# Performance work log

Hardware: AMD Instinct MI355X
Metric: run time of the kernel (lower is better)

## Reference

```python
import jax, jax.numpy as jnp
import numpy as np

N = 100000   # nodes
C = 128      # in_channels
K = 32       # n_super_nodes
B = 64       # graphs (num segments)


def setup_inputs() -> dict:
    key = jax.random.key(0)
    k_x, k_b, k_w1, k_b1, k_w2, k_b2 = jax.random.split(key, 6)
    x = jax.random.normal(k_x, (N, C), dtype=jnp.float32)
    batch = jnp.sort(jax.random.randint(k_b, (N,), 0, B))
    # assign_mlp params: Linear(C,C) -> ReLU -> Linear(C,K); stored as [in,out]
    W1 = jax.random.normal(k_w1, (C, C), dtype=jnp.float32) / np.sqrt(C)
    b1 = jax.random.normal(k_b1, (C,), dtype=jnp.float32) * 0.01
    W2 = jax.random.normal(k_w2, (C, K), dtype=jnp.float32) / np.sqrt(C)
    b2 = jax.random.normal(k_b2, (K,), dtype=jnp.float32) * 0.01
    return {"x": x, "batch": batch, "W1": W1, "b1": b1, "W2": W2, "b2": b2}


def reference(x, batch, W1, b1, W2, b2):
    # assignment logits: MLP over node features
    h = jax.nn.relu(x @ W1 + b1)          # [N, C]
    s = jax.nn.softmax(h @ W2 + b2, axis=-1)  # [N, K]
    # outer product per node, then scatter-sum by graph id
    x_expanded = x[:, None, :] * s[:, :, None]  # [N, K, C]
    out = jax.ops.segment_sum(x_expanded, batch, num_segments=B)  # [B, K, C]
    return (out, s)
```

## Files before the change

### kernel.cpp

```cpp
#include <hip/hip_runtime.h>
#include <hip/hip_bf16.h>

#define NN 100000
#define CC 128
#define KK 32
#define BB 64
#define CH 4
#define NCHUNK (NN / 32)
#define NSLOT 16

typedef __bf16 bf16x8 __attribute__((ext_vector_type(8)));
typedef float  f32x4  __attribute__((ext_vector_type(4)));

__device__ __forceinline__ unsigned short f2bf(float v) {
    union { __bf16 h; unsigned short s; } u;
    u.h = (__bf16)v;
    return u.s;
}
__device__ __forceinline__ float bf2f(unsigned short h) {
    union { unsigned u; float f; } a; a.u = ((unsigned)h) << 16;
    return a.f;
}
__device__ __forceinline__ void unpack_hilo(uint4 a, uint4 b,
                                            bf16x8& hi8, bf16x8& lo8) {
    union { unsigned u[4]; bf16x8 v; } H, L;
    H.u[0] = __builtin_amdgcn_perm(a.y, a.x, 0x05040100u);
    H.u[1] = __builtin_amdgcn_perm(a.w, a.z, 0x05040100u);
    H.u[2] = __builtin_amdgcn_perm(b.y, b.x, 0x05040100u);
    H.u[3] = __builtin_amdgcn_perm(b.w, b.z, 0x05040100u);
    L.u[0] = __builtin_amdgcn_perm(a.y, a.x, 0x07060302u);
    L.u[1] = __builtin_amdgcn_perm(a.w, a.z, 0x07060302u);
    L.u[2] = __builtin_amdgcn_perm(b.y, b.x, 0x07060302u);
    L.u[3] = __builtin_amdgcn_perm(b.w, b.z, 0x07060302u);
    hi8 = H.v; lo8 = L.v;
}

__global__ __launch_bounds__(256) void hp_prep(const int* __restrict__ batch,
                                               const float* __restrict__ W1,
                                               const float* __restrict__ W2,
                                               int* __restrict__ bounds,
                                               unsigned short* __restrict__ w1f,
                                               unsigned short* __restrict__ w2f,
                                               float* __restrict__ part) {
    if (blockIdx.x == 0 && threadIdx.x <= BB) {
        const int b = threadIdx.x;
        int lo = 0, hi = NN;
        while (lo < hi) {
            const int mid = (lo + hi) >> 1;
            if (batch[mid] < b) lo = mid + 1; else hi = mid;
        }
        bounds[b] = lo;
    }
    const int t = blockIdx.x * 256 + threadIdx.x;
    if (t < 16384) {
        const int idx  = t;
        const int j    = idx & 7;
        const int lane = (idx >> 3) & 63;
        const int nt   = (idx >> 9) & 7;
        const int kt   = idx >> 12;
        const int k = kt * 32 + (lane >> 4) * 8 + j;
        const int n = nt * 16 + (lane & 15);
        const float w = W1[k * CC + n];
        const unsigned short h = f2bf(w);
        w1f[idx]         = h;
        w1f[16384 + idx] = f2bf(w - bf2f(h));
    }
    if (t < 4096) {
        const int idx  = t;
        const int j    = idx & 7;
        const int lane = (idx >> 3) & 63;
        const int nt   = (idx >> 9) & 1;
        const int kt   = idx >> 10;
        const int k = kt * 32 + (lane >> 4) * 8 + j;
        const int n = nt * 16 + (lane & 15);
        const float w = W2[k * KK + n];
        const unsigned short h = f2bf(w);
        w2f[idx]        = h;
        w2f[4096 + idx] = f2bf(w - bf2f(h));
    }
    const float4 z = make_float4(0.f, 0.f, 0.f, 0.f);
    for (int i = t; i < BB * NSLOT * KK * CC / 4; i += 65536)
        *(float4*)(part + (size_t)i * 4) = z;
}

__global__ __launch_bounds__(256, 3) void hp_fused(
    const float* __restrict__ x,
    const unsigned short* __restrict__ w1f,
    const unsigned short* __restrict__ w2f,
    const float* __restrict__ b1,
    const float* __restrict__ b2,
    const int* __restrict__ batch,
    const int* __restrict__ bounds,
    float* __restrict__ s_out,
    float* __restrict__ part)
{
    __shared__ __align__(16) char uni[16896];
    __shared__ __align__(16) unsigned short xbL[8 * 64 * 8];
    __shared__ float lgT[32][36];
    __shared__ float redm[4][32];
    __shared__ float reds[4][32];

    unsigned short* xa   = (unsigned short*)uni;
    unsigned int*   hs16 = (unsigned int*)uni;

    const int t    = threadIdx.x;
    const int wave = __builtin_amdgcn_readfirstlane(t >> 6);
    const int lane = t & 63;

    const int pmt   = wave & 1;
    const int chalf = wave >> 1;
    const int nrow  = (lane >> 4) * 8;

    f32x4 pacc[4];
    #pragma unroll
    for (int i = 0; i < 4; ++i) pacc[i] = (f32x4){0.f, 0.f, 0.f, 0.f};

    int cg = __builtin_amdgcn_readfirstlane(batch[blockIdx.x * (CH * 32)]);

    auto flush = [&](int g) {
        const int slot = blockIdx.x - (bounds[g] >> 7);
        float* op = part + ((size_t)g * NSLOT + slot) * (KK * CC);
        #pragma unroll
        for (int i = 0; i < 4; ++i) {
            const int c = (chalf * 4 + i) * 16 + (lane & 15);
            #pragma unroll
            for (int r = 0; r < 4; ++r) {
                const int k = pmt * 16 + (lane >> 4) * 4 + r;
                op[k * CC + c] = pacc[i][r];
            }
            pacc[i] = (f32x4){0.f, 0.f, 0.f, 0.f};
        }
    };

    #pragma unroll 1
    for (int ch = 0; ch < CH; ++ch) {
        const int chunk = blockIdx.x * CH + ch;
        if (chunk >= NCHUNK) break;
        const int base = chunk * 32;

        __syncthreads();

        #pragma unroll
        for (int mt = 0; mt < 2; ++mt) {
            const int q  = mt * 4 + wave;
            const int n  = base + mt * 16 + (lane & 15);
            const int ck = wave * 32 + (lane >> 4) * 8;
            const float4 va = *(const float4*)(x + (size_t)n * CC + ck);
            const float4 vb = *(const float4*)(x + (size_t)n * CC + ck + 4);
            const float v[8] = {va.x, va.y, va.z, va.w, vb.x, vb.y, vb.z, vb.w};
            union { unsigned short s[8]; uint4 u; } H, L;
            #pragma unroll
            for (int j = 0; j < 8; ++j) {
                H.s[j] = f2bf(v[j]);
                L.s[j] = f2bf(v[j] - bf2f(H.s[j]));
            }
            unsigned short* d0 = xa + (q * 64 + lane) * 8;
            *(uint4*)(d0)        = H.u;
            *(uint4*)(d0 + 4096) = L.u;
        }

        #pragma unroll
        for (int cc = 0; cc < 2; ++cc) {
            const int ct = wave * 2 + cc;
            const int c  = ct * 16 + (lane & 15);
            const int nb = base + nrow;
            union { unsigned short s[8]; uint4 u; } Hb;
            #pragma unroll
            for (int j = 0; j < 8; ++j)
                Hb.s[j] = f2bf(x[(size_t)(nb + j) * CC + c]);
            *(uint4*)(xbL + ((size_t)ct * 64 + lane) * 8) = Hb.u;
        }
        __syncthreads();

        f32x4 acc[2][2];
        #pragma unroll
        for (int mt = 0; mt < 2; ++mt)
            #pragma unroll
            for (int nl = 0; nl < 2; ++nl)
                acc[mt][nl] = (f32x4){0.f, 0.f, 0.f, 0.f};

        #pragma unroll
        for (int kt = 0; kt < 4; ++kt) {
            bf16x8 ah[2], al[2];
            #pragma unroll
            for (int mt = 0; mt < 2; ++mt) {
                ah[mt] = *(const bf16x8*)(xa + ((mt * 4 + kt) * 64 + lane) * 8);
                al[mt] = *(const bf16x8*)(xa + 4096 + ((mt * 4 + kt) * 64 + lane) * 8);
            }
            #pragma unroll
            for (int nl = 0; nl < 2; ++nl) {
                const int nt = 2 * wave + nl;
                const bf16x8 wh = *(const bf16x8*)(w1f + ((kt * 8 + nt) * 64 + lane) * 8);
                const bf16x8 wl = *(const bf16x8*)(w1f + 16384 + ((kt * 8 + nt) * 64 + lane) * 8);
                #pragma unroll
                for (int mt = 0; mt < 2; ++mt) {
                    acc[mt][nl] = __builtin_amdgcn_mfma_f32_16x16x32_bf16(ah[mt], wh, acc[mt][nl], 0, 0, 0);
                    acc[mt][nl] = __builtin_amdgcn_mfma_f32_16x16x32_bf16(al[mt], wh, acc[mt][nl], 0, 0, 0);
                    acc[mt][nl] = __builtin_amdgcn_mfma_f32_16x16x32_bf16(ah[mt], wl, acc[mt][nl], 0, 0, 0);
                }
            }
        }
        __syncthreads();

        #pragma unroll
        for (int nl = 0; nl < 2; ++nl) {
            const int c = (2 * wave + nl) * 16 + (lane & 15);
            const float bv = b1[c];
            #pragma unroll
            for (int mt = 0; mt < 2; ++mt)
                #pragma unroll
                for (int r = 0; r < 4; ++r) {
                    const int node = mt * 16 + (lane >> 4) * 4 + r;
                    const float h = fmaxf(acc[mt][nl][r] + bv, 0.f);
                    const unsigned short hi = f2bf(h);
                    const unsigned short lo = f2bf(h - bf2f(hi));
                    hs16[node * 132 + c] = (unsigned)hi | ((unsigned)lo << 16);
                }
        }
        __syncthreads();

        {
            const int mt2 = wave & 1, nt2 = wave >> 1;
            f32x4 dacc = (f32x4){0.f, 0.f, 0.f, 0.f};
            #pragma unroll
            for (int kt = 0; kt < 4; ++kt) {
                const unsigned* hp = hs16 + (mt2 * 16 + (lane & 15)) * 132
                                          + kt * 32 + (lane >> 4) * 8;
                const uint4 u0 = *(const uint4*)hp;
                const uint4 u1 = *(const uint4*)(hp + 4);
                bf16x8 ah, al;
                unpack_hilo(u0, u1, ah, al);
                const bf16x8 wh = *(const bf16x8*)(w2f + ((kt * 2 + nt2) * 64 + lane) * 8);
                const bf16x8 wl = *(const bf16x8*)(w2f + 4096 + ((kt * 2 + nt2) * 64 + lane) * 8);
                dacc = __builtin_amdgcn_mfma_f32_16x16x32_bf16(ah, wh, dacc, 0, 0, 0);
                dacc = __builtin_amdgcn_mfma_f32_16x16x32_bf16(al, wh, dacc, 0, 0, 0);
                dacc = __builtin_amdgcn_mfma_f32_16x16x32_bf16(ah, wl, dacc, 0, 0, 0);
            }
            const int kcol = nt2 * 16 + (lane & 15);
            #pragma unroll
            for (int r = 0; r < 4; ++r) {
                const int node = mt2 * 16 + (lane >> 4) * 4 + r;
                lgT[node][kcol] = dacc[r];
            }
        }
        __syncthreads();

        {
            const int node = lane & 31;
            const int koff = ((lane >> 5) << 4) + wave * 4;
            const float4 bv2 = *(const float4*)(b2 + koff);
            const float4 lv  = *(const float4*)&lgT[node][koff];
            float lg[4] = {lv.x + bv2.x, lv.y + bv2.y, lv.z + bv2.z, lv.w + bv2.w};

            float m = fmaxf(fmaxf(lg[0], lg[1]), fmaxf(lg[2], lg[3]));
            m = fmaxf(m, __shfl_xor(m, 32));
            if (lane < 32) redm[wave][lane] = m;
            __syncthreads();
            const float M = fmaxf(fmaxf(redm[0][node], redm[1][node]),
                                  fmaxf(redm[2][node], redm[3][node]));
            const float e0 = __expf(lg[0] - M);
            const float e1 = __expf(lg[1] - M);
            const float e2 = __expf(lg[2] - M);
            const float e3 = __expf(lg[3] - M);
            float sp = (e0 + e1) + (e2 + e3);
            sp += __shfl_xor(sp, 32);
            if (lane < 32) reds[wave][lane] = sp;
            __syncthreads();
            const float S = (reds[0][node] + reds[1][node]) + (reds[2][node] + reds[3][node]);
            const float inv = 1.f / S;
            const float4 s4 = make_float4(e0 * inv, e1 * inv, e2 * inv, e3 * inv);
            *(float4*)(s_out + (size_t)(base + node) * KK + koff) = s4;
            *(float4*)&lgT[node][koff] = s4;
        }
        __syncthreads();

        {
            union { unsigned short s[8]; bf16x8 v; } A;
            const int kA = pmt * 16 + (lane & 15);
            #pragma unroll
            for (int j = 0; j < 8; ++j)
                A.s[j] = f2bf(lgT[nrow + j][kA]);
            bf16x8 Bv[4];
            #pragma unroll
            for (int i = 0; i < 4; ++i)
                Bv[i] = *(const bf16x8*)(xbL + ((size_t)(chalf * 4 + i) * 64 + lane) * 8);

            const int gl0 = __builtin_amdgcn_readfirstlane(batch[base]);
            const int gh  = __builtin_amdgcn_readfirstlane(batch[base + 31]);

            if (gl0 == cg && gh == cg) {
                #pragma unroll
                for (int i = 0; i < 4; ++i)
                    pacc[i] = __builtin_amdgcn_mfma_f32_16x16x32_bf16(A.v, Bv[i], pacc[i], 0, 0, 0);
            } else {
                int bt[8];
                #pragma unroll
                for (int j = 0; j < 8; ++j) bt[j] = batch[base + nrow + j];
                while (cg < gh) {
                    union { unsigned short s[8]; bf16x8 v; } Am;
                    #pragma unroll
                    for (int j = 0; j < 8; ++j)
                        Am.s[j] = (bt[j] == cg) ? A.s[j] : (unsigned short)0;
                    #pragma unroll
                    for (int i = 0; i < 4; ++i)
                        pacc[i] = __builtin_amdgcn_mfma_f32_16x16x32_bf16(Am.v, Bv[i], pacc[i], 0, 0, 0);
                    flush(cg);
                    ++cg;
                }
                union { unsigned short s[8]; bf16x8 v; } Am;
                #pragma unroll
                for (int j = 0; j < 8; ++j)
                    Am.s[j] = (bt[j] == cg) ? A.s[j] : (unsigned short)0;
                #pragma unroll
                for (int i = 0; i < 4; ++i)
                    pacc[i] = __builtin_amdgcn_mfma_f32_16x16x32_bf16(Am.v, Bv[i], pacc[i], 0, 0, 0);
            }
        }
    }

    flush(cg);
}

__global__ __launch_bounds__(256) void hp_reduce(const float* __restrict__ part,
                                                 float* __restrict__ out) {
    const int i = (blockIdx.x * 256 + threadIdx.x) * 4;
    if (i < BB * KK * CC) {
        const int b = i >> 12;
        const int j = i & 4095;
        const float* pp = part + (size_t)b * NSLOT * 4096 + j;
        float4 r = make_float4(0.f, 0.f, 0.f, 0.f);
        #pragma unroll 4
        for (int q = 0; q < NSLOT; ++q) {
            const float4 v = *(const float4*)(pp + (size_t)q * 4096);
            r.x += v.x; r.y += v.y; r.z += v.z; r.w += v.w;
        }
        *(float4*)(out + i) = r;
    }
}

extern "C" void kernel_launch(void* const* d_in, const int* in_sizes, int n_in,
                              void* d_out, int out_size, void* d_ws, size_t ws_size,
                              hipStream_t stream) {
    const float* x     = (const float*)d_in[0];
    const int*   batch = (const int*)d_in[1];
    const float* W1    = (const float*)d_in[2];
    const float* b1    = (const float*)d_in[3];
    const float* W2    = (const float*)d_in[4];
    const float* b2    = (const float*)d_in[5];

    float* out = (float*)d_out;
    float* s   = out + (size_t)BB * KK * CC;

    char* ws = (char*)d_ws;
    int*            bounds = (int*)ws;
    unsigned short* w1f    = (unsigned short*)(ws + 1024);
    unsigned short* w2f    = (unsigned short*)(ws + 66560);
    float*          part   = (float*)(ws + 82944);

    hp_prep<<<256, 256, 0, stream>>>(batch, W1, W2, bounds, w1f, w2f, part);
    const int nblk = (NCHUNK + CH - 1) / CH;
    hp_fused<<<nblk, 256, 0, stream>>>(x, w1f, w2f, b1, b2, batch, bounds, s, part);
    hp_reduce<<<BB * KK * CC / (256 * 4), 256, 0, stream>>>(part, out);
}
```

Measured before the change: 149.0 us.

## Process one 32-node chunk per block and reduce only touched partial slots

```diff
diff --git a/kernel.cpp b/kernel.cpp
--- a/kernel.cpp
+++ b/kernel.cpp
@@ -5,9 +5,8 @@
 #define CC 128
 #define KK 32
 #define BB 64
-#define CH 4
 #define NCHUNK (NN / 32)
-#define NSLOT 16
+#define NSLOT 64
 
 typedef __bf16 bf16x8 __attribute__((ext_vector_type(8)));
 typedef float  f32x4  __attribute__((ext_vector_type(4)));
@@ -40,8 +39,7 @@
                                                const float* __restrict__ W2,
                                                int* __restrict__ bounds,
                                                unsigned short* __restrict__ w1f,
-                                               unsigned short* __restrict__ w2f,
-                                               float* __restrict__ part) {
+                                               unsigned short* __restrict__ w2f) {
     if (blockIdx.x == 0 && threadIdx.x <= BB) {
         const int b = threadIdx.x;
         int lo = 0, hi = NN;
@@ -52,7 +50,7 @@
         bounds[b] = lo;
     }
     const int t = blockIdx.x * 256 + threadIdx.x;
-    if (t < 16384) {
+    {
         const int idx  = t;
         const int j    = idx & 7;
         const int lane = (idx >> 3) & 63;
@@ -78,9 +76,6 @@
         w2f[idx]        = h;
         w2f[4096 + idx] = f2bf(w - bf2f(h));
     }
-    const float4 z = make_float4(0.f, 0.f, 0.f, 0.f);
-    for (int i = t; i < BB * NSLOT * KK * CC / 4; i += 65536)
-        *(float4*)(part + (size_t)i * 4) = z;
 }
 
 __global__ __launch_bounds__(256, 3) void hp_fused(
@@ -111,14 +106,14 @@
     const int chalf = wave >> 1;
     const int nrow  = (lane >> 4) * 8;
 
+    const int base = blockIdx.x * 32;
+
     f32x4 pacc[4];
     #pragma unroll
     for (int i = 0; i < 4; ++i) pacc[i] = (f32x4){0.f, 0.f, 0.f, 0.f};
 
-    int cg = __builtin_amdgcn_readfirstlane(batch[blockIdx.x * (CH * 32)]);
-
     auto flush = [&](int g) {
-        const int slot = blockIdx.x - (bounds[g] >> 7);
+        const int slot = blockIdx.x - (bounds[g] >> 5);
         float* op = part + ((size_t)g * NSLOT + slot) * (KK * CC);
         #pragma unroll
         for (int i = 0; i < 4; ++i) {
@@ -132,181 +127,164 @@
         }
     };
 
-    #pragma unroll 1
-    for (int ch = 0; ch < CH; ++ch) {
-        const int chunk = blockIdx.x * CH + ch;
-        if (chunk >= NCHUNK) break;
-        const int base = chunk * 32;
-
+    #pragma unroll
+    for (int mt = 0; mt < 2; ++mt) {
+        const int q  = mt * 4 + wave;
+        const int n  = base + mt * 16 + (lane & 15);
+        const int ck = wave * 32 + (lane >> 4) * 8;
+        const float4 va = *(const float4*)(x + (size_t)n * CC + ck);
+        const float4 vb = *(const float4*)(x + (size_t)n * CC + ck + 4);
+        const float v[8] = {va.x, va.y, va.z, va.w, vb.x, vb.y, vb.z, vb.w};
+        union { unsigned short s[8]; uint4 u; } H, L;
+        #pragma unroll
+        for (int j = 0; j < 8; ++j) {
+            H.s[j] = f2bf(v[j]);
+            L.s[j] = f2bf(v[j] - bf2f(H.s[j]));
+        }
+        unsigned short* d0 = xa + (q * 64 + lane) * 8;
+        *(uint4*)(d0)        = H.u;
+        *(uint4*)(d0 + 4096) = L.u;
+    }
+
+    #pragma unroll
+    for (int cc = 0; cc < 2; ++cc) {
+        const int ct = wave * 2 + cc;
+        const int c  = ct * 16 + (lane & 15);
+        const int nb = base + nrow;
+        union { unsigned short s[8]; uint4 u; } Hb;
+        #pragma unroll
+        for (int j = 0; j < 8; ++j)
+            Hb.s[j] = f2bf(x[(size_t)(nb + j) * CC + c]);
+        *(uint4*)(xbL + ((size_t)ct * 64 + lane) * 8) = Hb.u;
+    }
+    __syncthreads();
+
+    f32x4 acc[2][2];
+    #pragma unroll
+    for (int mt = 0; mt < 2; ++mt)
+        #pragma unroll
+        for (int nl = 0; nl < 2; ++nl)
+            acc[mt][nl] = (f32x4){0.f, 0.f, 0.f, 0.f};
+
+    #pragma unroll
+    for (int kt = 0; kt < 4; ++kt) {
+        bf16x8 ah[2], al[2];
+        #pragma unroll
+        for (int mt = 0; mt < 2; ++mt) {
+            ah[mt] = *(const bf16x8*)(xa + ((mt * 4 + kt) * 64 + lane) * 8);
+            al[mt] = *(const bf16x8*)(xa + 4096 + ((mt * 4 + kt) * 64 + lane) * 8);
+        }
+        #pragma unroll
+        for (int nl = 0; nl < 2; ++nl) {
+            const int nt = 2 * wave + nl;
+            const bf16x8 wh = *(const bf16x8*)(w1f + ((kt * 8 + nt) * 64 + lane) * 8);
+            const bf16x8 wl = *(const bf16x8*)(w1f + 16384 + ((kt * 8 + nt) * 64 + lane) * 8);
+            #pragma unroll
+            for (int mt = 0; mt < 2; ++mt) {
+                acc[mt][nl] = __builtin_amdgcn_mfma_f32_16x16x32_bf16(ah[mt], wh, acc[mt][nl], 0, 0, 0);
+                acc[mt][nl] = __builtin_amdgcn_mfma_f32_16x16x32_bf16(al[mt], wh, acc[mt][nl], 0, 0, 0);
+                acc[mt][nl] = __builtin_amdgcn_mfma_f32_16x16x32_bf16(ah[mt], wl, acc[mt][nl], 0, 0, 0);
+            }
+        }
+    }
+    __syncthreads();
+
+    #pragma unroll
+    for (int nl = 0; nl < 2; ++nl) {
+        const int c = (2 * wave + nl) * 16 + (lane & 15);
+        const float bv = b1[c];
+        #pragma unroll
+        for (int mt = 0; mt < 2; ++mt)
+            #pragma unroll
+            for (int r = 0; r < 4; ++r) {
+                const int node = mt * 16 + (lane >> 4) * 4 + r;
+                const float h = fmaxf(acc[mt][nl][r] + bv, 0.f);
+                const unsigned short hi = f2bf(h);
+                const unsigned short lo = f2bf(h - bf2f(hi));
+                hs16[node * 132 + c] = (unsigned)hi | ((unsigned)lo << 16);
+            }
+    }
+    __syncthreads();
+
+    {
+        const int mt2 = wave & 1, nt2 = wave >> 1;
+        f32x4 dacc = (f32x4){0.f, 0.f, 0.f, 0.f};
+        #pragma unroll
+        for (int kt = 0; kt < 4; ++kt) {
+            const unsigned* hp = hs16 + (mt2 * 16 + (lane & 15)) * 132
+                                      + kt * 32 + (lane >> 4) * 8;
+            const uint4 u0 = *(const uint4*)hp;
+            const uint4 u1 = *(const uint4*)(hp + 4);
+            bf16x8 ah, al;
+            unpack_hilo(u0, u1, ah, al);
+            const bf16x8 wh = *(const bf16x8*)(w2f + ((kt * 2 + nt2) * 64 + lane) * 8);
+            const bf16x8 wl = *(const bf16x8*)(w2f + 4096 + ((kt * 2 + nt2) * 64 + lane) * 8);
+            dacc = __builtin_amdgcn_mfma_f32_16x16x32_bf16(ah, wh, dacc, 0, 0, 0);
+            dacc = __builtin_amdgcn_mfma_f32_16x16x32_bf16(al, wh, dacc, 0, 0, 0);
+            dacc = __builtin_amdgcn_mfma_f32_16x16x32_bf16(ah, wl, dacc, 0, 0, 0);
+        }
+        const int kcol = nt2 * 16 + (lane & 15);
+        #pragma unroll
+        for (int r = 0; r < 4; ++r) {
+            const int node = mt2 * 16 + (lane >> 4) * 4 + r;
+            lgT[node][kcol] = dacc[r];
+        }
+    }
+    __syncthreads();
+
+    {
+        const int node = lane & 31;
+        const int koff = ((lane >> 5) << 4) + wave * 4;
+        const float4 bv2 = *(const float4*)(b2 + koff);
+        const float4 lv  = *(const float4*)&lgT[node][koff];
+        float lg[4] = {lv.x + bv2.x, lv.y + bv2.y, lv.z + bv2.z, lv.w + bv2.w};
+
+        float m = fmaxf(fmaxf(lg[0], lg[1]), fmaxf(lg[2], lg[3]));
+        m = fmaxf(m, __shfl_xor(m, 32));
+        if (lane < 32) redm[wave][lane] = m;
         __syncthreads();
-
-        #pragma unroll
-        for (int mt = 0; mt < 2; ++mt) {
-            const int q  = mt * 4 + wave;
-            const int n  = base + mt * 16 + (lane & 15);
-            const int ck = wave * 32 + (lane >> 4) * 8;
-            const float4 va = *(const float4*)(x + (size_t)n * CC + ck);
-            const float4 vb = *(const float4*)(x + (size_t)n * CC + ck + 4);
-            const float v[8] = {va.x, va.y, va.z, va.w, vb.x, vb.y, vb.z, vb.w};
-            union { unsigned short s[8]; uint4 u; } H, L;
-            #pragma unroll
-            for (int j = 0; j < 8; ++j) {
-                H.s[j] = f2bf(v[j]);
-                L.s[j] = f2bf(v[j] - bf2f(H.s[j]));
-            }
-            unsigned short* d0 = xa + (q * 64 + lane) * 8;
-            *(uint4*)(d0)        = H.u;
-            *(uint4*)(d0 + 4096) = L.u;
-        }
-
-        #pragma unroll
-        for (int cc = 0; cc < 2; ++cc) {
-            const int ct = wave * 2 + cc;
-            const int c  = ct * 16 + (lane & 15);
-            const int nb = base + nrow;
-            union { unsigned short s[8]; uint4 u; } Hb;
-            #pragma unroll
-            for (int j = 0; j < 8; ++j)
-                Hb.s[j] = f2bf(x[(size_t)(nb + j) * CC + c]);
-            *(uint4*)(xbL + ((size_t)ct * 64 + lane) * 8) = Hb.u;
-        }
+        const float M = fmaxf(fmaxf(redm[0][node], redm[1][node]),
+                              fmaxf(redm[2][node], redm[3][node]));
+        const float e0 = __expf(lg[0] - M);
+        const float e1 = __expf(lg[1] - M);
+        const float e2 = __expf(lg[2] - M);
+        const float e3 = __expf(lg[3] - M);
+        float sp = (e0 + e1) + (e2 + e3);
+        sp += __shfl_xor(sp, 32);
+        if (lane < 32) reds[wave][lane] = sp;
         __syncthreads();
-
-        f32x4 acc[2][2];
-        #pragma unroll
-        for (int mt = 0; mt < 2; ++mt)
-            #pragma unroll
-            for (int nl = 0; nl < 2; ++nl)
-                acc[mt][nl] = (f32x4){0.f, 0.f, 0.f, 0.f};
-
-        #pragma unroll
-        for (int kt = 0; kt < 4; ++kt) {
-            bf16x8 ah[2], al[2];
-            #pragma unroll
-            for (int mt = 0; mt < 2; ++mt) {
-                ah[mt] = *(const bf16x8*)(xa + ((mt * 4 + kt) * 64 + lane) * 8);
-                al[mt] = *(const bf16x8*)(xa + 4096 + ((mt * 4 + kt) * 64 + lane) * 8);
-            }
-            #pragma unroll
-            for (int nl = 0; nl < 2; ++nl) {
-                const int nt = 2 * wave + nl;
-                const bf16x8 wh = *(const bf16x8*)(w1f + ((kt * 8 + nt) * 64 + lane) * 8);
-                const bf16x8 wl = *(const bf16x8*)(w1f + 16384 + ((kt * 8 + nt) * 64 + lane) * 8);
-                #pragma unroll
-                for (int mt = 0; mt < 2; ++mt) {
-                    acc[mt][nl] = __builtin_amdgcn_mfma_f32_16x16x32_bf16(ah[mt], wh, acc[mt][nl], 0, 0, 0);
-                    acc[mt][nl] = __builtin_amdgcn_mfma_f32_16x16x32_bf16(al[mt], wh, acc[mt][nl], 0, 0, 0);
-                    acc[mt][nl] = __builtin_amdgcn_mfma_f32_16x16x32_bf16(ah[mt], wl, acc[mt][nl], 0, 0, 0);
-                }
-            }
-        }
-        __syncthreads();
-
-        #pragma unroll
-        for (int nl = 0; nl < 2; ++nl) {
-            const int c = (2 * wave + nl) * 16 + (lane & 15);
-            const float bv = b1[c];
-            #pragma unroll
-            for (int mt = 0; mt < 2; ++mt)
-                #pragma unroll
-                for (int r = 0; r < 4; ++r) {
-                    const int node = mt * 16 + (lane >> 4) * 4 + r;
-                    const float h = fmaxf(acc[mt][nl][r] + bv, 0.f);
-                    const unsigned short hi = f2bf(h);
-                    const unsigned short lo = f2bf(h - bf2f(hi));
-                    hs16[node * 132 + c] = (unsigned)hi | ((unsigned)lo << 16);
-                }
-        }
-        __syncthreads();
-
-        {
-            const int mt2 = wave & 1, nt2 = wave >> 1;
-            f32x4 dacc = (f32x4){0.f, 0.f, 0.f, 0.f};
-            #pragma unroll
-            for (int kt = 0; kt < 4; ++kt) {
-                const unsigned* hp = hs16 + (mt2 * 16 + (lane & 15)) * 132
-                                          + kt * 32 + (lane >> 4) * 8;
-                const uint4 u0 = *(const uint4*)hp;
-                const uint4 u1 = *(const uint4*)(hp + 4);
-                bf16x8 ah, al;
-                unpack_hilo(u0, u1, ah, al);
-                const bf16x8 wh = *(const bf16x8*)(w2f + ((kt * 2 + nt2) * 64 + lane) * 8);
-                const bf16x8 wl = *(const bf16x8*)(w2f + 4096 + ((kt * 2 + nt2) * 64 + lane) * 8);
-                dacc = __builtin_amdgcn_mfma_f32_16x16x32_bf16(ah, wh, dacc, 0, 0, 0);
-                dacc = __builtin_amdgcn_mfma_f32_16x16x32_bf16(al, wh, dacc, 0, 0, 0);
-                dacc = __builtin_amdgcn_mfma_f32_16x16x32_bf16(ah, wl, dacc, 0, 0, 0);
-            }
-            const int kcol = nt2 * 16 + (lane & 15);
-            #pragma unroll
-            for (int r = 0; r < 4; ++r) {
-                const int node = mt2 * 16 + (lane >> 4) * 4 + r;
-                lgT[node][kcol] = dacc[r];
-            }
-        }
-        __syncthreads();
-
-        {
-            const int node = lane & 31;
-            const int koff = ((lane >> 5) << 4) + wave * 4;
-            const float4 bv2 = *(const float4*)(b2 + koff);
-            const float4 lv  = *(const float4*)&lgT[node][koff];
-            float lg[4] = {lv.x + bv2.x, lv.y + bv2.y, lv.z + bv2.z, lv.w + bv2.w};
-
-            float m = fmaxf(fmaxf(lg[0], lg[1]), fmaxf(lg[2], lg[3]));
-            m = fmaxf(m, __shfl_xor(m, 32));
-            if (lane < 32) redm[wave][lane] = m;
-            __syncthreads();
-            const float M = fmaxf(fmaxf(redm[0][node], redm[1][node]),
-                                  fmaxf(redm[2][node], redm[3][node]));
-            const float e0 = __expf(lg[0] - M);
-            const float e1 = __expf(lg[1] - M);
-            const float e2 = __expf(lg[2] - M);
-            const float e3 = __expf(lg[3] - M);
-            float sp = (e0 + e1) + (e2 + e3);
-            sp += __shfl_xor(sp, 32);
-            if (lane < 32) reds[wave][lane] = sp;
-            __syncthreads();
-            const float S = (reds[0][node] + reds[1][node]) + (reds[2][node] + reds[3][node]);
-            const float inv = 1.f / S;
-            const float4 s4 = make_float4(e0 * inv, e1 * inv, e2 * inv, e3 * inv);
-            *(float4*)(s_out + (size_t)(base + node) * KK + koff) = s4;
-            *(float4*)&lgT[node][koff] = s4;
-        }
-        __syncthreads();
-
-        {
-            union { unsigned short s[8]; bf16x8 v; } A;
-            const int kA = pmt * 16 + (lane & 15);
-            #pragma unroll
-            for (int j = 0; j < 8; ++j)
-                A.s[j] = f2bf(lgT[nrow + j][kA]);
-            bf16x8 Bv[4];
+        const float S = (reds[0][node] + reds[1][node]) + (reds[2][node] + reds[3][node]);
+        const float inv = 1.f / S;
+        const float4 s4 = make_float4(e0 * inv, e1 * inv, e2 * inv, e3 * inv);
+        *(float4*)(s_out + (size_t)(base + node) * KK + koff) = s4;
+        *(float4*)&lgT[node][koff] = s4;
+    }
+    __syncthreads();
+
+    {
+        union { unsigned short s[8]; bf16x8 v; } A;
+        const int kA = pmt * 16 + (lane & 15);
+        #pragma unroll
+        for (int j = 0; j < 8; ++j)
+            A.s[j] = f2bf(lgT[nrow + j][kA]);
+        bf16x8 Bv[4];
+        #pragma unroll
+        for (int i = 0; i < 4; ++i)
+            Bv[i] = *(const bf16x8*)(xbL + ((size_t)(chalf * 4 + i) * 64 + lane) * 8);
+
+        const int gl0 = __builtin_amdgcn_readfirstlane(batch[base]);
+        const int gh  = __builtin_amdgcn_readfirstlane(batch[base + 31]);
+        int cg = gl0;
+
+        if (gl0 == gh) {
             #pragma unroll
             for (int i = 0; i < 4; ++i)
-                Bv[i] = *(const bf16x8*)(xbL + ((size_t)(chalf * 4 + i) * 64 + lane) * 8);
-
-            const int gl0 = __builtin_amdgcn_readfirstlane(batch[base]);
-            const int gh  = __builtin_amdgcn_readfirstlane(batch[base + 31]);
-
-            if (gl0 == cg && gh == cg) {
-                #pragma unroll
-                for (int i = 0; i < 4; ++i)
-                    pacc[i] = __builtin_amdgcn_mfma_f32_16x16x32_bf16(A.v, Bv[i], pacc[i], 0, 0, 0);
-            } else {
-                int bt[8];
-                #pragma unroll
-                for (int j = 0; j < 8; ++j) bt[j] = batch[base + nrow + j];
-                while (cg < gh) {
-                    union { unsigned short s[8]; bf16x8 v; } Am;
-                    #pragma unroll
-                    for (int j = 0; j < 8; ++j)
-                        Am.s[j] = (bt[j] == cg) ? A.s[j] : (unsigned short)0;
-                    #pragma unroll
-                    for (int i = 0; i < 4; ++i)
-                        pacc[i] = __builtin_amdgcn_mfma_f32_16x16x32_bf16(Am.v, Bv[i], pacc[i], 0, 0, 0);
-                    flush(cg);
-                    ++cg;
-                }
+                pacc[i] = __builtin_amdgcn_mfma_f32_16x16x32_bf16(A.v, Bv[i], pacc[i], 0, 0, 0);
+        } else {
+            int bt[8];
+            #pragma unroll
+            for (int j = 0; j < 8; ++j) bt[j] = batch[base + nrow + j];
+            while (cg < gh) {
                 union { unsigned short s[8]; bf16x8 v; } Am;
                 #pragma unroll
                 for (int j = 0; j < 8; ++j)
@@ -314,28 +292,38 @@
                 #pragma unroll
                 for (int i = 0; i < 4; ++i)
                     pacc[i] = __builtin_amdgcn_mfma_f32_16x16x32_bf16(Am.v, Bv[i], pacc[i], 0, 0, 0);
+                flush(cg);
+                ++cg;
             }
-        }
-    }
-
-    flush(cg);
+            union { unsigned short s[8]; bf16x8 v; } Am;
+            #pragma unroll
+            for (int j = 0; j < 8; ++j)
+                Am.s[j] = (bt[j] == cg) ? A.s[j] : (unsigned short)0;
+            #pragma unroll
+            for (int i = 0; i < 4; ++i)
+                pacc[i] = __builtin_amdgcn_mfma_f32_16x16x32_bf16(Am.v, Bv[i], pacc[i], 0, 0, 0);
+        }
+
+        flush(cg);
+    }
 }
 
 __global__ __launch_bounds__(256) void hp_reduce(const float* __restrict__ part,
+                                                 const int* __restrict__ bounds,
                                                  float* __restrict__ out) {
-    const int i = (blockIdx.x * 256 + threadIdx.x) * 4;
-    if (i < BB * KK * CC) {
-        const int b = i >> 12;
-        const int j = i & 4095;
-        const float* pp = part + (size_t)b * NSLOT * 4096 + j;
-        float4 r = make_float4(0.f, 0.f, 0.f, 0.f);
-        #pragma unroll 4
-        for (int q = 0; q < NSLOT; ++q) {
-            const float4 v = *(const float4*)(pp + (size_t)q * 4096);
-            r.x += v.x; r.y += v.y; r.z += v.z; r.w += v.w;
-        }
-        *(float4*)(out + i) = r;
-    }
+    const int g = blockIdx.x >> 2;
+    const int q = blockIdx.x & 3;
+    const int j = q * 1024 + threadIdx.x * 4;
+    const int c0 = bounds[g] >> 5;
+    const int c1 = (bounds[g + 1] - 1) >> 5;
+    const int span = (bounds[g + 1] > bounds[g]) ? (c1 - c0 + 1) : 0;
+    const float* pp = part + (size_t)g * NSLOT * 4096 + j;
+    float4 r = make_float4(0.f, 0.f, 0.f, 0.f);
+    for (int s = 0; s < span; ++s) {
+        const float4 v = *(const float4*)(pp + (size_t)s * 4096);
+        r.x += v.x; r.y += v.y; r.z += v.z; r.w += v.w;
+    }
+    *(float4*)(out + (size_t)g * 4096 + j) = r;
 }
 
 extern "C" void kernel_launch(void* const* d_in, const int* in_sizes, int n_in,
@@ -357,8 +345,7 @@
     unsigned short* w2f    = (unsigned short*)(ws + 66560);
     float*          part   = (float*)(ws + 82944);
 
-    hp_prep<<<256, 256, 0, stream>>>(batch, W1, W2, bounds, w1f, w2f, part);
-    const int nblk = (NCHUNK + CH - 1) / CH;
-    hp_fused<<<nblk, 256, 0, stream>>>(x, w1f, w2f, b1, b2, batch, bounds, s, part);
-    hp_reduce<<<BB * KK * CC / (256 * 4), 256, 0, stream>>>(part, out);
-}
+    hp_prep<<<64, 256, 0, stream>>>(batch, W1, W2, bounds, w1f, w2f);
+    hp_fused<<<NCHUNK, 256, 0, stream>>>(x, w1f, w2f, b1, b2, batch, bounds, s, part);
+    hp_reduce<<<BB * 4, 256, 0, stream>>>(part, bounds, out);
+}
```

New measurement: 142.7 us. 1.04x faster.
